# Kernel optimization log

Measured on AMD Instinct MI355X. Metric: run time of the kernel, lower is better.

## Reference

```python
import jax, jax.numpy as jnp
import numpy as np

N_NODES = 100000
N_EDGES = 3200000
IN_DIM, HID_DIM, OUT_DIM = 384, 128, 5


def gcn_conv(x, src, dst, W, b, num_nodes):
    # PyG GCNConv: add self-loops, symmetric normalization, linear, aggregate, bias
    h = x @ W  # [N, out]
    ones = jnp.ones(src.shape[0], dtype=h.dtype)
    deg = jax.ops.segment_sum(ones, dst, num_segments=num_nodes)  # includes self-loops
    dinv = jnp.where(deg > 0, jax.lax.rsqrt(deg), 0.0)
    norm = dinv[src] * dinv[dst]  # [E+N]
    msg = h[src] * norm[:, None]
    out = jax.ops.segment_sum(msg, dst, num_segments=num_nodes)
    return out + b


def setup_inputs() -> dict:
    key = jax.random.key(0)
    ks = jax.random.split(key, 8)
    x = jax.random.normal(ks[0], (N_NODES, IN_DIM), dtype=jnp.float32)
    edge_index = jax.random.randint(ks[1], (2, N_EDGES), 0, N_NODES, dtype=jnp.int64)
    # Glorot-ish init for GCN linear weights
    def glorot(k, fi, fo):
        s = jnp.sqrt(6.0 / (fi + fo))
        return jax.random.uniform(k, (fi, fo), jnp.float32, -s, s)
    W1 = glorot(ks[2], IN_DIM, HID_DIM)
    b1 = jnp.zeros((HID_DIM,), jnp.float32)
    W2 = glorot(ks[3], HID_DIM, HID_DIM)
    b2 = jnp.zeros((HID_DIM,), jnp.float32)
    W3 = glorot(ks[4], HID_DIM, OUT_DIM)
    b3 = jnp.zeros((OUT_DIM,), jnp.float32)
    return {"x": x, "edge_index": edge_index, "W1": W1, "b1": b1,
            "W2": W2, "b2": b2, "W3": W3, "b3": b3}


def reference(x, edge_index, W1, b1, W2, b2, W3, b3):
    num_nodes = x.shape[0]
    loops = jnp.arange(num_nodes, dtype=edge_index.dtype)
    src = jnp.concatenate([edge_index[0], loops])
    dst = jnp.concatenate([edge_index[1], loops])
    # layer 1: GCNConv + ReLU (dropout is identity at inference)
    h = jax.nn.relu(gcn_conv(x, src, dst, W1, b1, num_nodes))
    # layer 2
    h = jax.nn.relu(gcn_conv(h, src, dst, W2, b2, num_nodes))
    # final layer: logits, no activation
    return gcn_conv(h, src, dst, W3, b3, num_nodes)
```

## Files before the change

### kernel.cpp

```cpp
#include <hip/hip_runtime.h>
#include <hip/hip_fp16.h>

#define NN 100000
#define NE 3200000
#define SCAN_CHUNK 1024

#define BSH 8
#define BKT_NODES 256
#define NBKT ((NN + BKT_NODES - 1) / BKT_NODES)
#define BIN_BLOCKS 256
#define EPB ((NE + BIN_BLOCKS - 1) / BIN_BLOCKS)
#define GH (NBKT * BIN_BLOCKS)
#define REC_CAP 9216

typedef unsigned int uint;
typedef unsigned short ushort;
typedef __attribute__((ext_vector_type(8))) _Float16 half8;
typedef __attribute__((ext_vector_type(4))) float f32x4;

__device__ inline void gload16(const void* g, void* l) {
    __builtin_amdgcn_global_load_lds(
        (const __attribute__((address_space(1))) void*)g,
        (__attribute__((address_space(3))) void*)l, 16, 0, 0);
}

__device__ inline uint f2h_pair(float a, float b) {
    return (uint)__half_as_ushort(__float2half(a)) |
           ((uint)__half_as_ushort(__float2half(b)) << 16);
}
__device__ inline float h2f_lo(uint u) { return __half2float(__ushort_as_half((ushort)(u & 0xFFFFu))); }
__device__ inline float h2f_hi(uint u) { return __half2float(__ushort_as_half((ushort)(u >> 16))); }
__device__ inline void splitH(float x, ushort& h, ushort& l) {
    __half hh = __float2half(x);
    h = __half_as_ushort(hh);
    l = __half_as_ushort(__float2half(x - __half2float(hh)));
}

__global__ __launch_bounds__(256) void hist_bkt(const int* __restrict__ dst,
                                                int* __restrict__ ghist) {
    __shared__ int h[NBKT];
    int t = threadIdx.x;
    for (int i = t; i < NBKT; i += 256) h[i] = 0;
    __syncthreads();
    int beg = blockIdx.x * EPB;
    int end = beg + EPB; if (end > NE) end = NE;
    for (int e = beg + t; e < end; e += 256)
        atomicAdd(&h[dst[e] >> BSH], 1);
    __syncthreads();
    for (int i = t; i < NBKT; i += 256)
        ghist[i * BIN_BLOCKS + blockIdx.x] = h[i];
}

__global__ __launch_bounds__(256) void scan_p1(const int* __restrict__ cnt,
                                               int* __restrict__ bsum, int N) {
    int t = threadIdx.x;
    int base = blockIdx.x * SCAN_CHUNK + t * 4;
    int s = 0;
#pragma unroll
    for (int q = 0; q < 4; q++) {
        int i = base + q;
        if (i < N) s += cnt[i];
    }
    __shared__ int red[4];
#pragma unroll
    for (int off = 32; off; off >>= 1) s += __shfl_down(s, off, 64);
    if ((t & 63) == 0) red[t >> 6] = s;
    __syncthreads();
    if (t == 0) bsum[blockIdx.x] = red[0] + red[1] + red[2] + red[3];
}

__global__ void scan_p2(int* __restrict__ bsum, int nb) {
    __shared__ int s[128];
    int t = threadIdx.x;
    int v = (t < nb) ? bsum[t] : 0;
    s[t] = v;
    __syncthreads();
    for (int off = 1; off < 128; off <<= 1) {
        int x = s[t];
        int add = (t >= off) ? s[t - off] : 0;
        __syncthreads();
        s[t] = x + add;
        __syncthreads();
    }
    if (t < nb) bsum[t] = s[t] - v;
}

__global__ __launch_bounds__(256) void scan_p3_plain(int* __restrict__ data,
                                                     const int* __restrict__ bsum, int N) {
    __shared__ int ts[256];
    int t = threadIdx.x;
    int base = blockIdx.x * SCAN_CHUNK + t * 4;
    int c[4];
    int s = 0;
#pragma unroll
    for (int q = 0; q < 4; q++) {
        int i = base + q;
        c[q] = (i < N) ? data[i] : 0;
        s += c[q];
    }
    ts[t] = s;
    __syncthreads();
    for (int off = 1; off < 256; off <<= 1) {
        int x = ts[t];
        int add = (t >= off) ? ts[t - off] : 0;
        __syncthreads();
        ts[t] = x + add;
        __syncthreads();
    }
    int run = bsum[blockIdx.x] + ts[t] - s;
#pragma unroll
    for (int q = 0; q < 4; q++) {
        int i = base + q;
        if (i < N) { data[i] = run; run += c[q]; }
    }
}

__global__ __launch_bounds__(256) void bin_edges(const int* __restrict__ src,
                                                 const int* __restrict__ dst,
                                                 const int* __restrict__ ghist,
                                                 uint* __restrict__ binned) {
    __shared__ int cur[NBKT];
    int t = threadIdx.x;
    for (int i = t; i < NBKT; i += 256) cur[i] = ghist[i * BIN_BLOCKS + blockIdx.x];
    __syncthreads();
    int beg = blockIdx.x * EPB;
    int end = beg + EPB; if (end > NE) end = NE;
    for (int e = beg + t; e < end; e += 256) {
        int d = dst[e];
        int b = d >> BSH;
        int p = atomicAdd(&cur[b], 1);
        binned[p] = ((uint)src[e] << BSH) | (uint)(d & (BKT_NODES - 1));
    }
}

__global__ __launch_bounds__(256) void bucket_csr(const uint* __restrict__ binned,
                                                  const int* __restrict__ ghist,
                                                  int* __restrict__ rowptr,
                                                  float* __restrict__ dinv,
                                                  int* __restrict__ col) {
    __shared__ uint rec[REC_CAP];
    __shared__ int c[BKT_NODES];
    __shared__ int ts[256];
    int t = threadIdx.x;
    int bkt = blockIdx.x;
    int beg = ghist[bkt * BIN_BLOCKS];
    int end = (bkt == NBKT - 1) ? NE : ghist[(bkt + 1) * BIN_BLOCKS];
    int n = end - beg;
    bool fits = (n <= REC_CAP);
    c[t] = 0;
    __syncthreads();
    if (fits) {
        for (int i = t; i < n; i += 256) {
            uint r = binned[beg + i];
            rec[i] = r;
            atomicAdd(&c[r & (BKT_NODES - 1)], 1);
        }
    } else {
        for (int j = beg + t; j < end; j += 256)
            atomicAdd(&c[binned[j] & (BKT_NODES - 1)], 1);
    }
    __syncthreads();
    int ci = c[t];
    ts[t] = ci;
    __syncthreads();
    for (int off = 1; off < 256; off <<= 1) {
        int x = ts[t];
        int add = (t >= off) ? ts[t - off] : 0;
        __syncthreads();
        ts[t] = x + add;
        __syncthreads();
    }
    int excl = ts[t] - ci;
    int node = bkt * BKT_NODES + t;
    if (node < NN) {
        rowptr[node] = beg + excl;
        dinv[node] = 1.0f / sqrtf((float)(ci + 1));
    }
    if (bkt == 0 && t == 0) rowptr[NN] = NE;
    __syncthreads();
    c[t] = beg + excl;
    __syncthreads();
    if (fits) {
        for (int i = t; i < n; i += 256) {
            uint r = rec[i];
            int p = atomicAdd(&c[r & (BKT_NODES - 1)], 1);
            col[p] = (int)(r >> BSH);
        }
    } else {
        for (int j = beg + t; j < end; j += 256) {
            uint r = binned[j];
            int p = atomicAdd(&c[r & (BKT_NODES - 1)], 1);
            col[p] = (int)(r >> BSH);
        }
    }
}

template <int K>
__global__ __launch_bounds__(256) void wsplit(const float* __restrict__ W,
                                              ushort* __restrict__ Wth,
                                              ushort* __restrict__ Wtl) {
    __shared__ float tile[32][128];
    int t = threadIdx.x;
    int kb = blockIdx.x;
    {
        int k = t >> 3, cq = t & 7;
#pragma unroll
        for (int q = 0; q < 4; q++) {
            float4 v = *(const float4*)&W[(size_t)(kb * 32 + k) * 128 + cq * 16 + q * 4];
            *(float4*)&tile[k][cq * 16 + q * 4] = v;
        }
    }
    __syncthreads();
    {
        int c = t >> 1, g = t & 1;
        ushort hs[16], ls[16];
#pragma unroll
        for (int i = 0; i < 16; i++) splitH(tile[g * 16 + i][c], hs[i], ls[i]);
        uint h[8], lo[8];
#pragma unroll
        for (int i = 0; i < 8; i++) {
            h[i] = (uint)hs[2 * i] | ((uint)hs[2 * i + 1] << 16);
            lo[i] = (uint)ls[2 * i] | ((uint)ls[2 * i + 1] << 16);
        }
        size_t o = (size_t)c * K + kb * 32 + g * 16;
        *(uint4*)&Wth[o] = make_uint4(h[0], h[1], h[2], h[3]);
        *(uint4*)&Wth[o + 8] = make_uint4(h[4], h[5], h[6], h[7]);
        *(uint4*)&Wtl[o] = make_uint4(lo[0], lo[1], lo[2], lo[3]);
        *(uint4*)&Wtl[o + 8] = make_uint4(lo[4], lo[5], lo[6], lo[7]);
    }
}

template <int K>
__global__ __launch_bounds__(256) void mfma_gemm_f32(const float* __restrict__ X,
                                                     const ushort* __restrict__ Wth,
                                                     const ushort* __restrict__ Wtl,
                                                     const float* __restrict__ dinv,
                                                     uint* __restrict__ Y, int M) {
    __shared__ char smem[24 * 1024];
    char* aP = smem;
    char* bH = smem + 8192;
    char* bL = smem + 16384;
    int tid = threadIdx.x;
    int w = tid >> 6, l = tid & 63;
    int rowBase = blockIdx.x * 128;

    f32x4 acc[2][8];
#pragma unroll
    for (int mf = 0; mf < 2; mf++)
#pragma unroll
        for (int n = 0; n < 8; n++) acc[mf][n] = (f32x4){0.f, 0.f, 0.f, 0.f};

    int sRow = tid >> 1, sKp = tid & 1;
    int gRow = rowBase + sRow;
    bool rowOK = gRow < M;
    size_t aBase = (size_t)(rowOK ? gRow : 0) * K + sKp * 16;

    float4 a0, a1, a2, a3;
    a0 = a1 = a2 = a3 = make_float4(0.f, 0.f, 0.f, 0.f);
    if (rowOK) {
        a0 = *(const float4*)&X[aBase];
        a1 = *(const float4*)&X[aBase + 4];
        a2 = *(const float4*)&X[aBase + 8];
        a3 = *(const float4*)&X[aBase + 12];
    }

    int fc = l & 15, fkg = l >> 4;
    int aoff0 = fkg * 2048 + ((2 * w + 0) * 16 + fc) * 16;
    int aoff1 = fkg * 2048 + ((2 * w + 1) * 16 + fc) * 16;

    for (int kt = 0; kt < K; kt += 32) {
#pragma unroll
        for (int i = 0; i < 2; i++) {
            int cb = (i * 4 + w) * 64;
            int c = cb + l;
            int kg = c >> 7, colb = c & 127;
            size_t go = (size_t)colb * K + kt + kg * 8;
            gload16(&Wth[go], bH + cb * 16);
            gload16(&Wtl[go], bL + cb * 16);
        }
        {
            float v[16] = {a0.x, a0.y, a0.z, a0.w, a1.x, a1.y, a1.z, a1.w,
                           a2.x, a2.y, a2.z, a2.w, a3.x, a3.y, a3.z, a3.w};
            uint hh[8];
#pragma unroll
            for (int i = 0; i < 8; i++) hh[i] = f2h_pair(v[2 * i], v[2 * i + 1]);
            *(uint4*)(aP + (2 * sKp) * 2048 + sRow * 16) = make_uint4(hh[0], hh[1], hh[2], hh[3]);
            *(uint4*)(aP + (2 * sKp + 1) * 2048 + sRow * 16) = make_uint4(hh[4], hh[5], hh[6], hh[7]);
        }
        __syncthreads();

        if (kt + 32 < K && rowOK) {
            size_t nb = aBase + kt + 32;
            a0 = *(const float4*)&X[nb];
            a1 = *(const float4*)&X[nb + 4];
            a2 = *(const float4*)&X[nb + 8];
            a3 = *(const float4*)&X[nb + 12];
        }

        half8 av0 = *(const half8*)(aP + aoff0);
        half8 av1 = *(const half8*)(aP + aoff1);
#pragma unroll
        for (int n = 0; n < 8; n++) {
            int boff = fkg * 2048 + (16 * n + fc) * 16;
            half8 bh = *(const half8*)(bH + boff);
            half8 bl = *(const half8*)(bL + boff);
            acc[0][n] = __builtin_amdgcn_mfma_f32_16x16x32_f16(av0, bh, acc[0][n], 0, 0, 0);
            acc[0][n] = __builtin_amdgcn_mfma_f32_16x16x32_f16(av0, bl, acc[0][n], 0, 0, 0);
            acc[1][n] = __builtin_amdgcn_mfma_f32_16x16x32_f16(av1, bh, acc[1][n], 0, 0, 0);
            acc[1][n] = __builtin_amdgcn_mfma_f32_16x16x32_f16(av1, bl, acc[1][n], 0, 0, 0);
        }
        __syncthreads();
    }

#pragma unroll
    for (int mf = 0; mf < 2; mf++) {
        float dscale[4];
#pragma unroll
        for (int r = 0; r < 4; r++) {
            int row = rowBase + (2 * w + mf) * 16 + fkg * 4 + r;
            dscale[r] = (row < M) ? dinv[row] : 0.f;
        }
#pragma unroll
        for (int n = 0; n < 8; n++) {
#pragma unroll
            for (int r = 0; r < 4; r++) {
                float val = acc[mf][n][r] * dscale[r];
                float p = __shfl_xor(val, 1, 64);
                int row = rowBase + (2 * w + mf) * 16 + fkg * 4 + r;
                if (!(l & 1) && row < M)
                    Y[(size_t)row * 64 + 8 * n + (fc >> 1)] = f2h_pair(val, p);
            }
        }
    }
}

__global__ __launch_bounds__(256) void mfma_gemm_f16(const ushort* __restrict__ Xh,
                                                     const ushort* __restrict__ Wth,
                                                     const ushort* __restrict__ Wtl,
                                                     const float* __restrict__ dinv,
                                                     uint* __restrict__ Y, int M) {
    __shared__ char smem[24 * 1024];
    char* aP = smem;
    char* bH = smem + 8192;
    char* bL = smem + 16384;
    int tid = threadIdx.x;
    int w = tid >> 6, l = tid & 63;
    int rowBase = blockIdx.x * 128;

    f32x4 acc[2][8];
#pragma unroll
    for (int mf = 0; mf < 2; mf++)
#pragma unroll
        for (int n = 0; n < 8; n++) acc[mf][n] = (f32x4){0.f, 0.f, 0.f, 0.f};

    int fc = l & 15, fkg = l >> 4;
    int aoff0 = fkg * 2048 + ((2 * w + 0) * 16 + fc) * 16;
    int aoff1 = fkg * 2048 + ((2 * w + 1) * 16 + fc) * 16;

    for (int kt = 0; kt < 128; kt += 32) {
#pragma unroll
        for (int i = 0; i < 2; i++) {
            int cb = (i * 4 + w) * 64;
            int c = cb + l;
            int kg = c >> 7, idx = c & 127;
            gload16(&Xh[(size_t)(rowBase + idx) * 128 + kt + kg * 8], aP + cb * 16);
            gload16(&Wth[(size_t)idx * 128 + kt + kg * 8], bH + cb * 16);
            gload16(&Wtl[(size_t)idx * 128 + kt + kg * 8], bL + cb * 16);
        }
        __syncthreads();
        half8 av0 = *(const half8*)(aP + aoff0);
        half8 av1 = *(const half8*)(aP + aoff1);
#pragma unroll
        for (int n = 0; n < 8; n++) {
            int boff = fkg * 2048 + (16 * n + fc) * 16;
            half8 bh = *(const half8*)(bH + boff);
            half8 bl = *(const half8*)(bL + boff);
            acc[0][n] = __builtin_amdgcn_mfma_f32_16x16x32_f16(av0, bh, acc[0][n], 0, 0, 0);
            acc[0][n] = __builtin_amdgcn_mfma_f32_16x16x32_f16(av0, bl, acc[0][n], 0, 0, 0);
            acc[1][n] = __builtin_amdgcn_mfma_f32_16x16x32_f16(av1, bh, acc[1][n], 0, 0, 0);
            acc[1][n] = __builtin_amdgcn_mfma_f32_16x16x32_f16(av1, bl, acc[1][n], 0, 0, 0);
        }
        __syncthreads();
    }

#pragma unroll
    for (int mf = 0; mf < 2; mf++) {
        float dscale[4];
#pragma unroll
        for (int r = 0; r < 4; r++) {
            int row = rowBase + (2 * w + mf) * 16 + fkg * 4 + r;
            dscale[r] = (row < M) ? dinv[row] : 0.f;
        }
#pragma unroll
        for (int n = 0; n < 8; n++) {
#pragma unroll
            for (int r = 0; r < 4; r++) {
                float val = acc[mf][n][r] * dscale[r];
                float p = __shfl_xor(val, 1, 64);
                int row = rowBase + (2 * w + mf) * 16 + fkg * 4 + r;
                if (!(l & 1) && row < M)
                    Y[(size_t)row * 64 + 8 * n + (fc >> 1)] = f2h_pair(val, p);
            }
        }
    }
}

__global__ __launch_bounds__(256) void gemm_n5h(const uint4* __restrict__ Xh,
                                                const float* __restrict__ W,
                                                const float* __restrict__ dinv,
                                                uint4* __restrict__ hc, int M) {
    __shared__ float wl[640];
    int t = threadIdx.x;
    for (int i = t; i < 640; i += 256) wl[i] = W[i];
    __syncthreads();
    int row = blockIdx.x * 256 + t;
    if (row >= M) return;
    float acc0 = 0.f, acc1 = 0.f, acc2 = 0.f, acc3 = 0.f, acc4 = 0.f;
#pragma unroll
    for (int kq = 0; kq < 16; kq++) {
        uint4 v = Xh[(size_t)row * 16 + kq];
        uint uu[4] = {v.x, v.y, v.z, v.w};
#pragma unroll
        for (int e = 0; e < 4; e++) {
            float x0 = h2f_lo(uu[e]);
            float x1 = h2f_hi(uu[e]);
            int k = kq * 8 + e * 2;
            acc0 = fmaf(x0, wl[k * 5 + 0], acc0); acc0 = fmaf(x1, wl[k * 5 + 5], acc0);
            acc1 = fmaf(x0, wl[k * 5 + 1], acc1); acc1 = fmaf(x1, wl[k * 5 + 6], acc1);
            acc2 = fmaf(x0, wl[k * 5 + 2], acc2); acc2 = fmaf(x1, wl[k * 5 + 7], acc2);
            acc3 = fmaf(x0, wl[k * 5 + 3], acc3); acc3 = fmaf(x1, wl[k * 5 + 8], acc3);
            acc4 = fmaf(x0, wl[k * 5 + 4], acc4); acc4 = fmaf(x1, wl[k * 5 + 9], acc4);
        }
    }
    float di = dinv[row];
    hc[row] = make_uint4(f2h_pair(acc0 * di, acc1 * di),
                         f2h_pair(acc2 * di, acc3 * di),
                         f2h_pair(acc4 * di, 0.f), 0u);
}

#define ACC8H(v)                              \
    a0 += h2f_lo(v.x); a1 += h2f_hi(v.x);     \
    a2 += h2f_lo(v.y); a3 += h2f_hi(v.y);     \
    a4 += h2f_lo(v.z); a5 += h2f_hi(v.z);     \
    a6 += h2f_lo(v.w); a7 += h2f_hi(v.w);

__global__ __launch_bounds__(256) void agg128_v3(const uint4* __restrict__ hb4,
                                                 const int* __restrict__ rowptr,
                                                 const int* __restrict__ col,
                                                 const float* __restrict__ dinv,
                                                 const float* __restrict__ bias,
                                                 uint4* __restrict__ out, int N, int do_relu) {
    int wave = threadIdx.x >> 6;
    int lane = threadIdx.x & 63;
    int node = blockIdx.x * 4 + wave;
    if (node >= N) return;
    int g = lane >> 4;
    int q = lane & 15;
    int beg = rowptr[node], end = rowptr[node + 1];
    float a0 = 0.f, a1 = 0.f, a2 = 0.f, a3 = 0.f, a4 = 0.f, a5 = 0.f, a6 = 0.f, a7 = 0.f;

    int j = beg;
    for (; j + 16 <= end; j += 16) {
        int s0 = col[j + g];
        int s1 = col[j + 4 + g];
        int s2 = col[j + 8 + g];
        int s3 = col[j + 12 + g];
        uint4 v0 = hb4[(size_t)s0 * 16 + q];
        uint4 v1 = hb4[(size_t)s1 * 16 + q];
        uint4 v2 = hb4[(size_t)s2 * 16 + q];
        uint4 v3 = hb4[(size_t)s3 * 16 + q];
        ACC8H(v0); ACC8H(v1); ACC8H(v2); ACC8H(v3);
    }
    if (j + 8 <= end) {
        int s0 = col[j + g];
        int s1 = col[j + 4 + g];
        uint4 v0 = hb4[(size_t)s0 * 16 + q];
        uint4 v1 = hb4[(size_t)s1 * 16 + q];
        ACC8H(v0); ACC8H(v1);
        j += 8;
    }
    if (j < end) {
        int jj0 = j + g, jj1 = j + 4 + g;
        bool p0 = jj0 < end, p1 = jj1 < end;
        int s0 = p0 ? col[jj0] : node;
        int s1 = p1 ? col[jj1] : node;
        uint4 v0 = hb4[(size_t)s0 * 16 + q];
        uint4 v1 = hb4[(size_t)s1 * 16 + q];
        if (!p0) v0 = make_uint4(0u, 0u, 0u, 0u);
        if (!p1) v1 = make_uint4(0u, 0u, 0u, 0u);
        ACC8H(v0); ACC8H(v1);
    }
#pragma unroll
    for (int off = 16; off <= 32; off <<= 1) {
        a0 += __shfl_xor(a0, off, 64);
        a1 += __shfl_xor(a1, off, 64);
        a2 += __shfl_xor(a2, off, 64);
        a3 += __shfl_xor(a3, off, 64);
        a4 += __shfl_xor(a4, off, 64);
        a5 += __shfl_xor(a5, off, 64);
        a6 += __shfl_xor(a6, off, 64);
        a7 += __shfl_xor(a7, off, 64);
    }
    if (g == 0) {
        uint4 vs = hb4[(size_t)node * 16 + q];
        ACC8H(vs);
        float di = dinv[node];
        const float4* bias4 = (const float4*)bias;
        float4 bb0 = bias4[q * 2], bb1 = bias4[q * 2 + 1];
        float o0 = a0 * di + bb0.x, o1 = a1 * di + bb0.y;
        float o2 = a2 * di + bb0.z, o3 = a3 * di + bb0.w;
        float o4 = a4 * di + bb1.x, o5 = a5 * di + bb1.y;
        float o6 = a6 * di + bb1.z, o7 = a7 * di + bb1.w;
        if (do_relu) {
            o0 = fmaxf(o0, 0.f); o1 = fmaxf(o1, 0.f);
            o2 = fmaxf(o2, 0.f); o3 = fmaxf(o3, 0.f);
            o4 = fmaxf(o4, 0.f); o5 = fmaxf(o5, 0.f);
            o6 = fmaxf(o6, 0.f); o7 = fmaxf(o7, 0.f);
        }
        out[(size_t)node * 16 + q] =
            make_uint4(f2h_pair(o0, o1), f2h_pair(o2, o3), f2h_pair(o4, o5), f2h_pair(o6, o7));
    }
}

__global__ void agg5_v2(const uint4* __restrict__ hc, const int* __restrict__ rowptr,
                        const int* __restrict__ col, const float* __restrict__ dinv,
                        const float* __restrict__ b3, float* __restrict__ out, int N) {
    int node = blockIdx.x * 256 + threadIdx.x;
    if (node >= N) return;
    float a0 = 0.f, a1 = 0.f, a2 = 0.f, a3 = 0.f, a4 = 0.f;
    int beg = rowptr[node], end = rowptr[node + 1];
#pragma unroll 2
    for (int j = beg; j < end; ++j) {
        uint4 v = hc[col[j]];
        a0 += h2f_lo(v.x); a1 += h2f_hi(v.x);
        a2 += h2f_lo(v.y); a3 += h2f_hi(v.y);
        a4 += h2f_lo(v.z);
    }
    uint4 vs = hc[node];
    a0 += h2f_lo(vs.x); a1 += h2f_hi(vs.x);
    a2 += h2f_lo(vs.y); a3 += h2f_hi(vs.y);
    a4 += h2f_lo(vs.z);
    float di = dinv[node];
    out[node * 5 + 0] = a0 * di + b3[0];
    out[node * 5 + 1] = a1 * di + b3[1];
    out[node * 5 + 2] = a2 * di + b3[2];
    out[node * 5 + 3] = a3 * di + b3[3];
    out[node * 5 + 4] = a4 * di + b3[4];
}

static inline size_t align512(size_t x) { return (x + 511) & ~(size_t)511; }

extern "C" void kernel_launch(void* const* d_in, const int* in_sizes, int n_in,
                              void* d_out, int out_size, void* d_ws, size_t ws_size,
                              hipStream_t stream) {
    const float* x  = (const float*)d_in[0];
    const int* ei   = (const int*)d_in[1];
    const float* W1 = (const float*)d_in[2];
    const float* b1 = (const float*)d_in[3];
    const float* W2 = (const float*)d_in[4];
    const float* b2 = (const float*)d_in[5];
    const float* W3 = (const float*)d_in[6];
    const float* b3 = (const float*)d_in[7];
    const int* src = ei;
    const int* dst = ei + NE;

    char* ws = (char*)d_ws;
    size_t off = 0;
    int* rowptr = (int*)(ws + off);     off += align512((size_t)(NN + 1) * 4);
    float* dinv = (float*)(ws + off);   off += align512((size_t)NN * 4);
    int* bsum = (int*)(ws + off);       off += align512((size_t)128 * 4);
    int* ghist = (int*)(ws + off);      off += align512((size_t)GH * 4);
    ushort* wt1h = (ushort*)(ws + off); off += align512((size_t)128 * 384 * 2);
    ushort* wt1l = (ushort*)(ws + off); off += align512((size_t)128 * 384 * 2);
    ushort* wt2h = (ushort*)(ws + off); off += align512((size_t)128 * 128 * 2);
    ushort* wt2l = (ushort*)(ws + off); off += align512((size_t)128 * 128 * 2);
    int* col = (int*)(ws + off);        off += align512((size_t)NE * 4);
    uint* hb = (uint*)(ws + off);       off += align512((size_t)NN * 64 * 4);
    char* bufF = (char*)(ws + off);     off += align512((size_t)NN * 128 * 4);
    uint4* hc = (uint4*)(ws + off);     off += align512((size_t)NN * 16);
    uint* binned = (uint*)bufF;
    (void)ws_size;

    wsplit<384><<<12, 256, 0, stream>>>(W1, wt1h, wt1l);
    wsplit<128><<<4, 256, 0, stream>>>(W2, wt2h, wt2l);

    hist_bkt<<<BIN_BLOCKS, 256, 0, stream>>>(dst, ghist);
    {
        int nb = (GH + SCAN_CHUNK - 1) / SCAN_CHUNK;
        scan_p1<<<nb, 256, 0, stream>>>(ghist, bsum, GH);
        scan_p2<<<1, 128, 0, stream>>>(bsum, nb);
        scan_p3_plain<<<nb, 256, 0, stream>>>(ghist, bsum, GH);
    }
    bin_edges<<<BIN_BLOCKS, 256, 0, stream>>>(src, dst, ghist, binned);
    bucket_csr<<<NBKT, 256, 0, stream>>>(binned, ghist, rowptr, dinv, col);

    int gemm_blocks = (NN + 127) / 128;
    mfma_gemm_f32<384><<<gemm_blocks, 256, 0, stream>>>(x, wt1h, wt1l, dinv, hb, NN);
    agg128_v3<<<(NN + 3) / 4, 256, 0, stream>>>((const uint4*)hb, rowptr, col, dinv, b1,
                                                (uint4*)bufF, NN, 1);
    mfma_gemm_f16<<<gemm_blocks, 256, 0, stream>>>((const ushort*)bufF, wt2h, wt2l, dinv, hb, NN);
    agg128_v3<<<(NN + 3) / 4, 256, 0, stream>>>((const uint4*)hb, rowptr, col, dinv, b2,
                                                (uint4*)bufF, NN, 1);
    gemm_n5h<<<(NN + 255) / 256, 256, 0, stream>>>((const uint4*)bufF, W3, dinv, hc, NN);
    agg5_v2<<<(NN + 255) / 256, 256, 0, stream>>>(hc, rowptr, col, dinv, b3, (float*)d_out, NN);
}
```

Baseline: 439.6 us.

## Fuse layer-2 aggregation with layer-3 projection and wave-parallelize final aggregation

The second 128-wide aggregation now applies bias and ReLU and then immediately projects onto W3 in registers, using a shuffle reduction across the 16 lanes, so it writes the 5-wide hc directly. This drops the fp16 128-wide intermediate write/read and the separate gemm_n5h launch. The final 5-wide aggregation moves from one thread per node to one wave per node with lane-strided edges and a shuffle reduction, which balances load across edges. The cost is that all four lane groups now run the epilogue's projection math, and the final pass launches many more threads.

```diff
diff --git a/kernel.cpp b/kernel.cpp
--- a/kernel.cpp
+++ b/kernel.cpp
@@ -405,51 +405,62 @@
     }
 }
 
-__global__ __launch_bounds__(256) void gemm_n5h(const uint4* __restrict__ Xh,
-                                                const float* __restrict__ W,
-                                                const float* __restrict__ dinv,
-                                                uint4* __restrict__ hc, int M) {
-    __shared__ float wl[640];
-    int t = threadIdx.x;
-    for (int i = t; i < 640; i += 256) wl[i] = W[i];
-    __syncthreads();
-    int row = blockIdx.x * 256 + t;
-    if (row >= M) return;
-    float acc0 = 0.f, acc1 = 0.f, acc2 = 0.f, acc3 = 0.f, acc4 = 0.f;
-#pragma unroll
-    for (int kq = 0; kq < 16; kq++) {
-        uint4 v = Xh[(size_t)row * 16 + kq];
-        uint uu[4] = {v.x, v.y, v.z, v.w};
-#pragma unroll
-        for (int e = 0; e < 4; e++) {
-            float x0 = h2f_lo(uu[e]);
-            float x1 = h2f_hi(uu[e]);
-            int k = kq * 8 + e * 2;
-            acc0 = fmaf(x0, wl[k * 5 + 0], acc0); acc0 = fmaf(x1, wl[k * 5 + 5], acc0);
-            acc1 = fmaf(x0, wl[k * 5 + 1], acc1); acc1 = fmaf(x1, wl[k * 5 + 6], acc1);
-            acc2 = fmaf(x0, wl[k * 5 + 2], acc2); acc2 = fmaf(x1, wl[k * 5 + 7], acc2);
-            acc3 = fmaf(x0, wl[k * 5 + 3], acc3); acc3 = fmaf(x1, wl[k * 5 + 8], acc3);
-            acc4 = fmaf(x0, wl[k * 5 + 4], acc4); acc4 = fmaf(x1, wl[k * 5 + 9], acc4);
-        }
-    }
-    float di = dinv[row];
-    hc[row] = make_uint4(f2h_pair(acc0 * di, acc1 * di),
-                         f2h_pair(acc2 * di, acc3 * di),
-                         f2h_pair(acc4 * di, 0.f), 0u);
-}
-
 #define ACC8H(v)                              \
     a0 += h2f_lo(v.x); a1 += h2f_hi(v.x);     \
     a2 += h2f_lo(v.y); a3 += h2f_hi(v.y);     \
     a4 += h2f_lo(v.z); a5 += h2f_hi(v.z);     \
     a6 += h2f_lo(v.w); a7 += h2f_hi(v.w);
 
+#define AGG_GATHER_BODY                                            \
+    int j = beg;                                                   \
+    for (; j + 16 <= end; j += 16) {                               \
+        int s0 = col[j + g];                                       \
+        int s1 = col[j + 4 + g];                                   \
+        int s2 = col[j + 8 + g];                                   \
+        int s3 = col[j + 12 + g];                                  \
+        uint4 v0 = hb4[(size_t)s0 * 16 + q];                       \
+        uint4 v1 = hb4[(size_t)s1 * 16 + q];                       \
+        uint4 v2 = hb4[(size_t)s2 * 16 + q];                       \
+        uint4 v3 = hb4[(size_t)s3 * 16 + q];                       \
+        ACC8H(v0); ACC8H(v1); ACC8H(v2); ACC8H(v3);                \
+    }                                                              \
+    if (j + 8 <= end) {                                            \
+        int s0 = col[j + g];                                       \
+        int s1 = col[j + 4 + g];                                   \
+        uint4 v0 = hb4[(size_t)s0 * 16 + q];                       \
+        uint4 v1 = hb4[(size_t)s1 * 16 + q];                       \
+        ACC8H(v0); ACC8H(v1);                                      \
+        j += 8;                                                    \
+    }                                                              \
+    if (j < end) {                                                 \
+        int jj0 = j + g, jj1 = j + 4 + g;                          \
+        bool p0 = jj0 < end, p1 = jj1 < end;                       \
+        int s0 = p0 ? col[jj0] : node;                             \
+        int s1 = p1 ? col[jj1] : node;                             \
+        uint4 v0 = hb4[(size_t)s0 * 16 + q];                       \
+        uint4 v1 = hb4[(size_t)s1 * 16 + q];                       \
+        if (!p0) v0 = make_uint4(0u, 0u, 0u, 0u);                  \
+        if (!p1) v1 = make_uint4(0u, 0u, 0u, 0u);                  \
+        ACC8H(v0); ACC8H(v1);                                      \
+    }                                                              \
+    _Pragma("unroll")                                              \
+    for (int off = 16; off <= 32; off <<= 1) {                     \
+        a0 += __shfl_xor(a0, off, 64);                             \
+        a1 += __shfl_xor(a1, off, 64);                             \
+        a2 += __shfl_xor(a2, off, 64);                             \
+        a3 += __shfl_xor(a3, off, 64);                             \
+        a4 += __shfl_xor(a4, off, 64);                             \
+        a5 += __shfl_xor(a5, off, 64);                             \
+        a6 += __shfl_xor(a6, off, 64);                             \
+        a7 += __shfl_xor(a7, off, 64);                             \
+    }
+
 __global__ __launch_bounds__(256) void agg128_v3(const uint4* __restrict__ hb4,
                                                  const int* __restrict__ rowptr,
                                                  const int* __restrict__ col,
                                                  const float* __restrict__ dinv,
                                                  const float* __restrict__ bias,
-                                                 uint4* __restrict__ out, int N, int do_relu) {
+                                                 uint4* __restrict__ out, int N) {
     int wave = threadIdx.x >> 6;
     int lane = threadIdx.x & 63;
     int node = blockIdx.x * 4 + wave;
@@ -458,94 +469,115 @@
     int q = lane & 15;
     int beg = rowptr[node], end = rowptr[node + 1];
     float a0 = 0.f, a1 = 0.f, a2 = 0.f, a3 = 0.f, a4 = 0.f, a5 = 0.f, a6 = 0.f, a7 = 0.f;
-
-    int j = beg;
-    for (; j + 16 <= end; j += 16) {
-        int s0 = col[j + g];
-        int s1 = col[j + 4 + g];
-        int s2 = col[j + 8 + g];
-        int s3 = col[j + 12 + g];
-        uint4 v0 = hb4[(size_t)s0 * 16 + q];
-        uint4 v1 = hb4[(size_t)s1 * 16 + q];
-        uint4 v2 = hb4[(size_t)s2 * 16 + q];
-        uint4 v3 = hb4[(size_t)s3 * 16 + q];
-        ACC8H(v0); ACC8H(v1); ACC8H(v2); ACC8H(v3);
-    }
-    if (j + 8 <= end) {
-        int s0 = col[j + g];
-        int s1 = col[j + 4 + g];
-        uint4 v0 = hb4[(size_t)s0 * 16 + q];
-        uint4 v1 = hb4[(size_t)s1 * 16 + q];
-        ACC8H(v0); ACC8H(v1);
-        j += 8;
-    }
-    if (j < end) {
-        int jj0 = j + g, jj1 = j + 4 + g;
-        bool p0 = jj0 < end, p1 = jj1 < end;
-        int s0 = p0 ? col[jj0] : node;
-        int s1 = p1 ? col[jj1] : node;
-        uint4 v0 = hb4[(size_t)s0 * 16 + q];
-        uint4 v1 = hb4[(size_t)s1 * 16 + q];
-        if (!p0) v0 = make_uint4(0u, 0u, 0u, 0u);
-        if (!p1) v1 = make_uint4(0u, 0u, 0u, 0u);
-        ACC8H(v0); ACC8H(v1);
-    }
-#pragma unroll
-    for (int off = 16; off <= 32; off <<= 1) {
-        a0 += __shfl_xor(a0, off, 64);
-        a1 += __shfl_xor(a1, off, 64);
-        a2 += __shfl_xor(a2, off, 64);
-        a3 += __shfl_xor(a3, off, 64);
-        a4 += __shfl_xor(a4, off, 64);
-        a5 += __shfl_xor(a5, off, 64);
-        a6 += __shfl_xor(a6, off, 64);
-        a7 += __shfl_xor(a7, off, 64);
-    }
+    AGG_GATHER_BODY
     if (g == 0) {
         uint4 vs = hb4[(size_t)node * 16 + q];
         ACC8H(vs);
         float di = dinv[node];
         const float4* bias4 = (const float4*)bias;
         float4 bb0 = bias4[q * 2], bb1 = bias4[q * 2 + 1];
-        float o0 = a0 * di + bb0.x, o1 = a1 * di + bb0.y;
-        float o2 = a2 * di + bb0.z, o3 = a3 * di + bb0.w;
-        float o4 = a4 * di + bb1.x, o5 = a5 * di + bb1.y;
-        float o6 = a6 * di + bb1.z, o7 = a7 * di + bb1.w;
-        if (do_relu) {
-            o0 = fmaxf(o0, 0.f); o1 = fmaxf(o1, 0.f);
-            o2 = fmaxf(o2, 0.f); o3 = fmaxf(o3, 0.f);
-            o4 = fmaxf(o4, 0.f); o5 = fmaxf(o5, 0.f);
-            o6 = fmaxf(o6, 0.f); o7 = fmaxf(o7, 0.f);
-        }
+        float o0 = fmaxf(a0 * di + bb0.x, 0.f), o1 = fmaxf(a1 * di + bb0.y, 0.f);
+        float o2 = fmaxf(a2 * di + bb0.z, 0.f), o3 = fmaxf(a3 * di + bb0.w, 0.f);
+        float o4 = fmaxf(a4 * di + bb1.x, 0.f), o5 = fmaxf(a5 * di + bb1.y, 0.f);
+        float o6 = fmaxf(a6 * di + bb1.z, 0.f), o7 = fmaxf(a7 * di + bb1.w, 0.f);
         out[(size_t)node * 16 + q] =
             make_uint4(f2h_pair(o0, o1), f2h_pair(o2, o3), f2h_pair(o4, o5), f2h_pair(o6, o7));
     }
 }
 
-__global__ void agg5_v2(const uint4* __restrict__ hc, const int* __restrict__ rowptr,
-                        const int* __restrict__ col, const float* __restrict__ dinv,
-                        const float* __restrict__ b3, float* __restrict__ out, int N) {
-    int node = blockIdx.x * 256 + threadIdx.x;
+__global__ __launch_bounds__(256) void agg128_proj(const uint4* __restrict__ hb4,
+                                                   const int* __restrict__ rowptr,
+                                                   const int* __restrict__ col,
+                                                   const float* __restrict__ dinv,
+                                                   const float* __restrict__ bias,
+                                                   const float* __restrict__ W3,
+                                                   uint4* __restrict__ hc, int N) {
+    __shared__ float wl[640];
+    int t = threadIdx.x;
+    for (int i = t; i < 640; i += 256) wl[i] = W3[i];
+    __syncthreads();
+    int wave = t >> 6;
+    int lane = t & 63;
+    int node = blockIdx.x * 4 + wave;
     if (node >= N) return;
+    int g = lane >> 4;
+    int q = lane & 15;
+    int beg = rowptr[node], end = rowptr[node + 1];
+    float a0 = 0.f, a1 = 0.f, a2 = 0.f, a3 = 0.f, a4 = 0.f, a5 = 0.f, a6 = 0.f, a7 = 0.f;
+    AGG_GATHER_BODY
+    uint4 vs = hb4[(size_t)node * 16 + q];
+    ACC8H(vs);
+    float di = dinv[node];
+    const float4* bias4 = (const float4*)bias;
+    float4 bb0 = bias4[q * 2], bb1 = bias4[q * 2 + 1];
+    float o[8];
+    o[0] = fmaxf(a0 * di + bb0.x, 0.f); o[1] = fmaxf(a1 * di + bb0.y, 0.f);
+    o[2] = fmaxf(a2 * di + bb0.z, 0.f); o[3] = fmaxf(a3 * di + bb0.w, 0.f);
+    o[4] = fmaxf(a4 * di + bb1.x, 0.f); o[5] = fmaxf(a5 * di + bb1.y, 0.f);
+    o[6] = fmaxf(a6 * di + bb1.z, 0.f); o[7] = fmaxf(a7 * di + bb1.w, 0.f);
+    float p0 = 0.f, p1 = 0.f, p2 = 0.f, p3 = 0.f, p4 = 0.f;
+#pragma unroll
+    for (int i = 0; i < 8; i++) {
+        const float* wr = &wl[(q * 8 + i) * 5];
+        p0 = fmaf(o[i], wr[0], p0);
+        p1 = fmaf(o[i], wr[1], p1);
+        p2 = fmaf(o[i], wr[2], p2);
+        p3 = fmaf(o[i], wr[3], p3);
+        p4 = fmaf(o[i], wr[4], p4);
+    }
+#pragma unroll
+    for (int off = 1; off <= 8; off <<= 1) {
+        p0 += __shfl_xor(p0, off, 64);
+        p1 += __shfl_xor(p1, off, 64);
+        p2 += __shfl_xor(p2, off, 64);
+        p3 += __shfl_xor(p3, off, 64);
+        p4 += __shfl_xor(p4, off, 64);
+    }
+    if (lane == 0)
+        hc[node] = make_uint4(f2h_pair(p0 * di, p1 * di), f2h_pair(p2 * di, p3 * di),
+                              f2h_pair(p4 * di, 0.f), 0u);
+}
+
+__global__ __launch_bounds__(256) void agg5_wave(const uint4* __restrict__ hc,
+                                                 const int* __restrict__ rowptr,
+                                                 const int* __restrict__ col,
+                                                 const float* __restrict__ dinv,
+                                                 const float* __restrict__ b3,
+                                                 float* __restrict__ out, int N) {
+    int wave = threadIdx.x >> 6;
+    int lane = threadIdx.x & 63;
+    int node = blockIdx.x * 4 + wave;
+    if (node >= N) return;
+    int beg = rowptr[node], end = rowptr[node + 1];
     float a0 = 0.f, a1 = 0.f, a2 = 0.f, a3 = 0.f, a4 = 0.f;
-    int beg = rowptr[node], end = rowptr[node + 1];
-#pragma unroll 2
-    for (int j = beg; j < end; ++j) {
+    for (int j = beg + lane; j < end; j += 64) {
         uint4 v = hc[col[j]];
         a0 += h2f_lo(v.x); a1 += h2f_hi(v.x);
         a2 += h2f_lo(v.y); a3 += h2f_hi(v.y);
         a4 += h2f_lo(v.z);
     }
-    uint4 vs = hc[node];
-    a0 += h2f_lo(vs.x); a1 += h2f_hi(vs.x);
-    a2 += h2f_lo(vs.y); a3 += h2f_hi(vs.y);
-    a4 += h2f_lo(vs.z);
-    float di = dinv[node];
-    out[node * 5 + 0] = a0 * di + b3[0];
-    out[node * 5 + 1] = a1 * di + b3[1];
-    out[node * 5 + 2] = a2 * di + b3[2];
-    out[node * 5 + 3] = a3 * di + b3[3];
-    out[node * 5 + 4] = a4 * di + b3[4];
+    if (lane == 0) {
+        uint4 vs = hc[node];
+        a0 += h2f_lo(vs.x); a1 += h2f_hi(vs.x);
+        a2 += h2f_lo(vs.y); a3 += h2f_hi(vs.y);
+        a4 += h2f_lo(vs.z);
+    }
+#pragma unroll
+    for (int off = 1; off <= 32; off <<= 1) {
+        a0 += __shfl_xor(a0, off, 64);
+        a1 += __shfl_xor(a1, off, 64);
+        a2 += __shfl_xor(a2, off, 64);
+        a3 += __shfl_xor(a3, off, 64);
+        a4 += __shfl_xor(a4, off, 64);
+    }
+    if (lane == 0) {
+        float di = dinv[node];
+        out[node * 5 + 0] = a0 * di + b3[0];
+        out[node * 5 + 1] = a1 * di + b3[1];
+        out[node * 5 + 2] = a2 * di + b3[2];
+        out[node * 5 + 3] = a3 * di + b3[3];
+        out[node * 5 + 4] = a4 * di + b3[4];
+    }
 }
 
 static inline size_t align512(size_t x) { return (x + 511) & ~(size_t)511; }
@@ -597,10 +629,9 @@
     int gemm_blocks = (NN + 127) / 128;
     mfma_gemm_f32<384><<<gemm_blocks, 256, 0, stream>>>(x, wt1h, wt1l, dinv, hb, NN);
     agg128_v3<<<(NN + 3) / 4, 256, 0, stream>>>((const uint4*)hb, rowptr, col, dinv, b1,
-                                                (uint4*)bufF, NN, 1);
+                                                (uint4*)bufF, NN);
     mfma_gemm_f16<<<gemm_blocks, 256, 0, stream>>>((const ushort*)bufF, wt2h, wt2l, dinv, hb, NN);
-    agg128_v3<<<(NN + 3) / 4, 256, 0, stream>>>((const uint4*)hb, rowptr, col, dinv, b2,
-                                                (uint4*)bufF, NN, 1);
-    gemm_n5h<<<(NN + 255) / 256, 256, 0, stream>>>((const uint4*)bufF, W3, dinv, hc, NN);
-    agg5_v2<<<(NN + 255) / 256, 256, 0, stream>>>(hc, rowptr, col, dinv, b3, (float*)d_out, NN);
-}
+    agg128_proj<<<(NN + 3) / 4, 256, 0, stream>>>((const uint4*)hb, rowptr, col, dinv, b2, W3,
+                                                  hc, NN);
+    agg5_wave<<<(NN + 3) / 4, 256, 0, stream>>>(hc, rowptr, col, dinv, b3, (float*)d_out, NN);
+}
```

Measured after the change: 439.7 us. About the same (+0.0%).

## Store hidden features in 16-column slices and aggregate per slice

Applied to the files above, without the earlier changes.

Hidden features move from row-major [N,128] fp16 to eight column slices of [N,16], each 3.2 MB. The GEMM epilogues, GEMM A-loads and the layer-3 projection are rewritten for this layout, and the aggregation kernel now runs one block per (node group, slice). The goal is to make each slice's random gather hit L2 far more often than gathering from the full 25.6 MB table. In exchange, each gather is only 8 bytes per lane, so column indices are read eight times and there are many more small accesses and blocks.

```diff
diff --git a/kernel.cpp b/kernel.cpp
--- a/kernel.cpp
+++ b/kernel.cpp
@@ -328,7 +328,7 @@
                 float p = __shfl_xor(val, 1, 64);
                 int row = rowBase + (2 * w + mf) * 16 + fkg * 4 + r;
                 if (!(l & 1) && row < M)
-                    Y[(size_t)row * 64 + 8 * n + (fc >> 1)] = f2h_pair(val, p);
+                    Y[(size_t)n * (NN * 8) + (size_t)row * 8 + (fc >> 1)] = f2h_pair(val, p);
             }
         }
     }
@@ -363,7 +363,9 @@
             int cb = (i * 4 + w) * 64;
             int c = cb + l;
             int kg = c >> 7, idx = c & 127;
-            gload16(&Xh[(size_t)(rowBase + idx) * 128 + kt + kg * 8], aP + cb * 16);
+            int d = kt + kg * 8;
+            int sl = d >> 4, dd = d & 15;
+            gload16(&Xh[(size_t)sl * (NN * 16) + (size_t)(rowBase + idx) * 16 + dd], aP + cb * 16);
             gload16(&Wth[(size_t)idx * 128 + kt + kg * 8], bH + cb * 16);
             gload16(&Wtl[(size_t)idx * 128 + kt + kg * 8], bL + cb * 16);
         }
@@ -399,13 +401,13 @@
                 float p = __shfl_xor(val, 1, 64);
                 int row = rowBase + (2 * w + mf) * 16 + fkg * 4 + r;
                 if (!(l & 1) && row < M)
-                    Y[(size_t)row * 64 + 8 * n + (fc >> 1)] = f2h_pair(val, p);
+                    Y[(size_t)n * (NN * 8) + (size_t)row * 8 + (fc >> 1)] = f2h_pair(val, p);
             }
         }
     }
 }
 
-__global__ __launch_bounds__(256) void gemm_n5h(const uint4* __restrict__ Xh,
+__global__ __launch_bounds__(256) void gemm_n5h(const uint4* __restrict__ Xh4,
                                                 const float* __restrict__ W,
                                                 const float* __restrict__ dinv,
                                                 uint4* __restrict__ hc, int M) {
@@ -418,7 +420,7 @@
     float acc0 = 0.f, acc1 = 0.f, acc2 = 0.f, acc3 = 0.f, acc4 = 0.f;
 #pragma unroll
     for (int kq = 0; kq < 16; kq++) {
-        uint4 v = Xh[(size_t)row * 16 + kq];
+        uint4 v = Xh4[(size_t)(kq >> 1) * (NN * 2) + (size_t)row * 2 + (kq & 1)];
         uint uu[4] = {v.x, v.y, v.z, v.w};
 #pragma unroll
         for (int e = 0; e < 4; e++) {
@@ -438,87 +440,71 @@
                          f2h_pair(acc4 * di, 0.f), 0u);
 }
 
-#define ACC8H(v)                              \
-    a0 += h2f_lo(v.x); a1 += h2f_hi(v.x);     \
-    a2 += h2f_lo(v.y); a3 += h2f_hi(v.y);     \
-    a4 += h2f_lo(v.z); a5 += h2f_hi(v.z);     \
-    a6 += h2f_lo(v.w); a7 += h2f_hi(v.w);
-
-__global__ __launch_bounds__(256) void agg128_v3(const uint4* __restrict__ hb4,
+__global__ __launch_bounds__(256) void agg128_sl(const uint2* __restrict__ hb2,
                                                  const int* __restrict__ rowptr,
                                                  const int* __restrict__ col,
                                                  const float* __restrict__ dinv,
                                                  const float* __restrict__ bias,
-                                                 uint4* __restrict__ out, int N, int do_relu) {
+                                                 uint2* __restrict__ out, int N, int do_relu) {
+    int slice = blockIdx.x & 7;
+    int nb = blockIdx.x >> 3;
     int wave = threadIdx.x >> 6;
     int lane = threadIdx.x & 63;
-    int node = blockIdx.x * 4 + wave;
+    int node = nb * 4 + wave;
     if (node >= N) return;
-    int g = lane >> 4;
-    int q = lane & 15;
+    int g = lane >> 2;
+    int q = lane & 3;
+    size_t sbase = (size_t)slice * (N * 4);
     int beg = rowptr[node], end = rowptr[node + 1];
-    float a0 = 0.f, a1 = 0.f, a2 = 0.f, a3 = 0.f, a4 = 0.f, a5 = 0.f, a6 = 0.f, a7 = 0.f;
+    float a0 = 0.f, a1 = 0.f, a2 = 0.f, a3 = 0.f;
 
     int j = beg;
-    for (; j + 16 <= end; j += 16) {
+    for (; j + 32 <= end; j += 32) {
         int s0 = col[j + g];
-        int s1 = col[j + 4 + g];
-        int s2 = col[j + 8 + g];
-        int s3 = col[j + 12 + g];
-        uint4 v0 = hb4[(size_t)s0 * 16 + q];
-        uint4 v1 = hb4[(size_t)s1 * 16 + q];
-        uint4 v2 = hb4[(size_t)s2 * 16 + q];
-        uint4 v3 = hb4[(size_t)s3 * 16 + q];
-        ACC8H(v0); ACC8H(v1); ACC8H(v2); ACC8H(v3);
-    }
-    if (j + 8 <= end) {
+        int s1 = col[j + 16 + g];
+        uint2 v0 = hb2[sbase + (size_t)s0 * 4 + q];
+        uint2 v1 = hb2[sbase + (size_t)s1 * 4 + q];
+        a0 += h2f_lo(v0.x); a1 += h2f_hi(v0.x);
+        a2 += h2f_lo(v0.y); a3 += h2f_hi(v0.y);
+        a0 += h2f_lo(v1.x); a1 += h2f_hi(v1.x);
+        a2 += h2f_lo(v1.y); a3 += h2f_hi(v1.y);
+    }
+    if (j + 16 <= end) {
         int s0 = col[j + g];
-        int s1 = col[j + 4 + g];
-        uint4 v0 = hb4[(size_t)s0 * 16 + q];
-        uint4 v1 = hb4[(size_t)s1 * 16 + q];
-        ACC8H(v0); ACC8H(v1);
-        j += 8;
+        uint2 v0 = hb2[sbase + (size_t)s0 * 4 + q];
+        a0 += h2f_lo(v0.x); a1 += h2f_hi(v0.x);
+        a2 += h2f_lo(v0.y); a3 += h2f_hi(v0.y);
+        j += 16;
     }
     if (j < end) {
-        int jj0 = j + g, jj1 = j + 4 + g;
-        bool p0 = jj0 < end, p1 = jj1 < end;
-        int s0 = p0 ? col[jj0] : node;
-        int s1 = p1 ? col[jj1] : node;
-        uint4 v0 = hb4[(size_t)s0 * 16 + q];
-        uint4 v1 = hb4[(size_t)s1 * 16 + q];
-        if (!p0) v0 = make_uint4(0u, 0u, 0u, 0u);
-        if (!p1) v1 = make_uint4(0u, 0u, 0u, 0u);
-        ACC8H(v0); ACC8H(v1);
-    }
-#pragma unroll
-    for (int off = 16; off <= 32; off <<= 1) {
+        int jj = j + g;
+        bool p = jj < end;
+        int s0 = p ? col[jj] : node;
+        uint2 v0 = hb2[sbase + (size_t)s0 * 4 + q];
+        if (!p) v0 = make_uint2(0u, 0u);
+        a0 += h2f_lo(v0.x); a1 += h2f_hi(v0.x);
+        a2 += h2f_lo(v0.y); a3 += h2f_hi(v0.y);
+    }
+#pragma unroll
+    for (int off = 4; off <= 32; off <<= 1) {
         a0 += __shfl_xor(a0, off, 64);
         a1 += __shfl_xor(a1, off, 64);
         a2 += __shfl_xor(a2, off, 64);
         a3 += __shfl_xor(a3, off, 64);
-        a4 += __shfl_xor(a4, off, 64);
-        a5 += __shfl_xor(a5, off, 64);
-        a6 += __shfl_xor(a6, off, 64);
-        a7 += __shfl_xor(a7, off, 64);
     }
     if (g == 0) {
-        uint4 vs = hb4[(size_t)node * 16 + q];
-        ACC8H(vs);
+        uint2 vs = hb2[sbase + (size_t)node * 4 + q];
+        a0 += h2f_lo(vs.x); a1 += h2f_hi(vs.x);
+        a2 += h2f_lo(vs.y); a3 += h2f_hi(vs.y);
         float di = dinv[node];
-        const float4* bias4 = (const float4*)bias;
-        float4 bb0 = bias4[q * 2], bb1 = bias4[q * 2 + 1];
-        float o0 = a0 * di + bb0.x, o1 = a1 * di + bb0.y;
-        float o2 = a2 * di + bb0.z, o3 = a3 * di + bb0.w;
-        float o4 = a4 * di + bb1.x, o5 = a5 * di + bb1.y;
-        float o6 = a6 * di + bb1.z, o7 = a7 * di + bb1.w;
+        float4 bb = ((const float4*)bias)[slice * 4 + q];
+        float o0 = a0 * di + bb.x, o1 = a1 * di + bb.y;
+        float o2 = a2 * di + bb.z, o3 = a3 * di + bb.w;
         if (do_relu) {
             o0 = fmaxf(o0, 0.f); o1 = fmaxf(o1, 0.f);
             o2 = fmaxf(o2, 0.f); o3 = fmaxf(o3, 0.f);
-            o4 = fmaxf(o4, 0.f); o5 = fmaxf(o5, 0.f);
-            o6 = fmaxf(o6, 0.f); o7 = fmaxf(o7, 0.f);
-        }
-        out[(size_t)node * 16 + q] =
-            make_uint4(f2h_pair(o0, o1), f2h_pair(o2, o3), f2h_pair(o4, o5), f2h_pair(o6, o7));
+        }
+        out[sbase + (size_t)node * 4 + q] = make_uint2(f2h_pair(o0, o1), f2h_pair(o2, o3));
     }
 }
 
@@ -595,12 +581,13 @@
     bucket_csr<<<NBKT, 256, 0, stream>>>(binned, ghist, rowptr, dinv, col);
 
     int gemm_blocks = (NN + 127) / 128;
+    int agg_blocks = 8 * ((NN + 3) / 4);
     mfma_gemm_f32<384><<<gemm_blocks, 256, 0, stream>>>(x, wt1h, wt1l, dinv, hb, NN);
-    agg128_v3<<<(NN + 3) / 4, 256, 0, stream>>>((const uint4*)hb, rowptr, col, dinv, b1,
-                                                (uint4*)bufF, NN, 1);
+    agg128_sl<<<agg_blocks, 256, 0, stream>>>((const uint2*)hb, rowptr, col, dinv, b1,
+                                              (uint2*)bufF, NN, 1);
     mfma_gemm_f16<<<gemm_blocks, 256, 0, stream>>>((const ushort*)bufF, wt2h, wt2l, dinv, hb, NN);
-    agg128_v3<<<(NN + 3) / 4, 256, 0, stream>>>((const uint4*)hb, rowptr, col, dinv, b2,
-                                                (uint4*)bufF, NN, 1);
+    agg128_sl<<<agg_blocks, 256, 0, stream>>>((const uint2*)hb, rowptr, col, dinv, b2,
+                                              (uint2*)bufF, NN, 1);
     gemm_n5h<<<(NN + 255) / 256, 256, 0, stream>>>((const uint4*)bufF, W3, dinv, hc, NN);
     agg5_v2<<<(NN + 255) / 256, 256, 0, stream>>>(hc, rowptr, col, dinv, b3, (float*)d_out, NN);
 }
```

Result: slower. 705.2 us (+60.4%).
